# Kernel tuning notes

Measured on AMD Instinct MI355X. Metric: run time of the kernel, lower is better.

The kernel has to match this reference:

```python
import jax, jax.numpy as jnp
import numpy as np

N_NODES = 100000
N_EDGES = 1600000
IN_CH = 128
OUT_CH = 128


def setup_inputs() -> dict:
    key = jax.random.key(0)
    k1, k2, k3, k4, k5, k6 = jax.random.split(key, 6)
    x = jax.random.normal(k1, (N_NODES, IN_CH), dtype=jnp.float32)
    weight = jax.random.normal(k2, (IN_CH, OUT_CH), dtype=jnp.float32) * (1.0 / np.sqrt(IN_CH))
    bias = jax.random.uniform(k3, (OUT_CH,), dtype=jnp.float32)
    edge_row = jax.random.randint(k4, (N_EDGES,), 0, N_NODES, dtype=jnp.int64)
    edge_col = jax.random.randint(k5, (N_EDGES,), 0, N_NODES, dtype=jnp.int64)
    edge_weight = jax.random.uniform(k6, (N_EDGES,), dtype=jnp.float32)
    return {"x": x, "weight": weight, "bias": bias,
            "edge_row": edge_row, "edge_col": edge_col, "edge_weight": edge_weight}


def reference(x, weight, bias, edge_row, edge_col, edge_weight):
    # Dense transform: [N, in] @ [in, out] -> [N, out]
    h = x @ weight
    # SpMM: out[r] = sum_e w_e * h[c_e] for edges (r, c) -- gather + scatter-add
    msgs = edge_weight[:, None] * h[edge_col]          # [E, out]
    agg = jax.ops.segment_sum(msgs, edge_row, num_segments=N_NODES)  # [N, out]
    return agg + bias
```

## Files before the change

kernel.cpp:

```cpp
#include <hip/hip_runtime.h>

#define N_NODES 100000
#define N_EDGES_MAX 1600000
#define IN_CH 128
#define OUT_CH 128
#define NB 391
#define BLK_E 2048
#define NBLK_P 800
#define CAP_LDS 5120

typedef __attribute__((ext_vector_type(8))) short bf16x8_t;
typedef __attribute__((ext_vector_type(4))) float f32x4_t;

constexpr size_t align_up(size_t x) { return (x + 255) & ~size_t(255); }
constexpr size_t H_OFF     = 0;
constexpr size_t H_SZ      = (size_t)N_NODES * OUT_CH * 2;
constexpr size_t BREC_OFF  = align_up(H_OFF + H_SZ);
constexpr size_t BREC_SZ   = (size_t)N_EDGES_MAX * 8;
constexpr size_t SREC_OFF  = align_up(BREC_OFF + BREC_SZ);
constexpr size_t BLK_OFF   = align_up(SREC_OFF + BREC_SZ);
constexpr size_t BLK_SZ    = (size_t)NB * NBLK_P * 4;
constexpr size_t BTOT_OFF  = align_up(BLK_OFF + BLK_SZ);
constexpr size_t BTOT_SZ   = (size_t)NB * 4;
constexpr size_t BBASE_OFF = align_up(BTOT_OFF + BTOT_SZ);
constexpr size_t BBASE_SZ  = (size_t)(NB + 1) * 4;
constexpr size_t RS_OFF    = align_up(BBASE_OFF + BBASE_SZ);
constexpr size_t RS_SZ     = (size_t)(N_NODES + 1) * 4;
constexpr size_t WS_NEED   = RS_OFF + RS_SZ;

__device__ __forceinline__ unsigned short f2bf(float f) {
    unsigned u = __float_as_uint(f);
    return (unsigned short)((u + 0x7FFFu + ((u >> 16) & 1u)) >> 16);
}
__device__ __forceinline__ float bf2f(unsigned short b) {
    return __uint_as_float((unsigned)b << 16);
}
__device__ __forceinline__ float bflo(unsigned u) { return __uint_as_float(u << 16); }
__device__ __forceinline__ float bfhi(unsigned u) { return __uint_as_float(u & 0xFFFF0000u); }

__device__ __forceinline__ void accum8(float4& a0, float4& a1, const uint4 hv,
                                       const float wt) {
    a0.x += wt * bflo(hv.x); a0.y += wt * bfhi(hv.x);
    a0.z += wt * bflo(hv.y); a0.w += wt * bfhi(hv.y);
    a1.x += wt * bflo(hv.z); a1.y += wt * bfhi(hv.z);
    a1.z += wt * bflo(hv.w); a1.w += wt * bfhi(hv.w);
}

__global__ __launch_bounds__(256) void gemm_mfma(const float* __restrict__ x,
                                                 const float* __restrict__ W,
                                                 unsigned short* __restrict__ h) {
    __shared__ unsigned short WTl[128 * 136];
    const int t = threadIdx.x;

    const float4* W4 = (const float4*)W;
#pragma unroll
    for (int i = 0; i < 16; ++i) {
        const int idx = t + 256 * i;
        float4 v = W4[idx];
        const int base = idx * 4;
        const int k = base >> 7;
        const int c = base & 127;
        WTl[(c + 0) * 136 + k] = f2bf(v.x);
        WTl[(c + 1) * 136 + k] = f2bf(v.y);
        WTl[(c + 2) * 136 + k] = f2bf(v.z);
        WTl[(c + 3) * 136 + k] = f2bf(v.w);
    }
    __syncthreads();

    const int wv = t >> 6;
    const int l  = t & 63;
    const int lr = l & 15;
    const int lk = (l >> 4) * 8;
    const long rbase = (long)blockIdx.x * 64 + wv * 16;

    f32x4_t acc[8];
#pragma unroll
    for (int i = 0; i < 8; ++i) acc[i] = (f32x4_t){0.f, 0.f, 0.f, 0.f};

    long arow = rbase + lr;
    if (arow >= N_NODES) arow = N_NODES - 1;
    const float4* xr = (const float4*)(x + arow * IN_CH);

    for (int kc = 0; kc < 128; kc += 32) {
        float4 f0 = xr[(kc + lk) >> 2];
        float4 f1 = xr[((kc + lk) >> 2) + 1];
        bf16x8_t a;
        a[0] = (short)f2bf(f0.x); a[1] = (short)f2bf(f0.y);
        a[2] = (short)f2bf(f0.z); a[3] = (short)f2bf(f0.w);
        a[4] = (short)f2bf(f1.x); a[5] = (short)f2bf(f1.y);
        a[6] = (short)f2bf(f1.z); a[7] = (short)f2bf(f1.w);
#pragma unroll
        for (int ct = 0; ct < 8; ++ct) {
            bf16x8_t b = *(const bf16x8_t*)&WTl[(ct * 16 + lr) * 136 + kc + lk];
            acc[ct] = __builtin_amdgcn_mfma_f32_16x16x32_bf16(a, b, acc[ct], 0, 0, 0);
        }
    }

    const int r0 = (l >> 4) * 4;
#pragma unroll
    for (int ct = 0; ct < 8; ++ct) {
        const int col = ct * 16 + lr;
#pragma unroll
        for (int reg = 0; reg < 4; ++reg) {
            long r = rbase + r0 + reg;
            if (r < N_NODES) h[r * OUT_CH + col] = f2bf(acc[ct][reg]);
        }
    }
}

__global__ __launch_bounds__(256) void bucket_hist(const int* __restrict__ erow,
                                                   unsigned* __restrict__ blkcnt,
                                                   int n) {
    __shared__ unsigned cnt[NB];
    const int t = threadIdx.x, p = blockIdx.x;
    for (int i = t; i < NB; i += 256) cnt[i] = 0u;
    __syncthreads();
    const int e0 = p * BLK_E;
#pragma unroll
    for (int j = 0; j < 8; ++j) {
        int e = e0 + j * 256 + t;
        if (e < n) atomicAdd(&cnt[(unsigned)erow[e] >> 8], 1u);
    }
    __syncthreads();
    for (int i = t; i < NB; i += 256) blkcnt[(size_t)i * NBLK_P + p] = cnt[i];
}

__global__ __launch_bounds__(256) void scan_col(unsigned* __restrict__ blkcnt,
                                                unsigned* __restrict__ btotal,
                                                int nblk) {
    __shared__ unsigned part[256];
    const int b = blockIdx.x, t = threadIdx.x;
    unsigned* col = blkcnt + (size_t)b * NBLK_P;
    unsigned v[4];
    unsigned sum = 0;
    const int p0 = t * 4;
#pragma unroll
    for (int j = 0; j < 4; ++j) {
        int p = p0 + j;
        v[j] = (p < nblk) ? col[p] : 0u;
        sum += v[j];
    }
    part[t] = sum;
    __syncthreads();
    for (int off = 1; off < 256; off <<= 1) {
        unsigned a = (t >= off) ? part[t - off] : 0u;
        __syncthreads();
        part[t] += a;
        __syncthreads();
    }
    unsigned excl = part[t] - sum;
#pragma unroll
    for (int j = 0; j < 4; ++j) {
        int p = p0 + j;
        if (p < nblk) { unsigned tv = v[j]; col[p] = excl; excl += tv; }
    }
    if (t == 255) btotal[b] = part[255];
}

__global__ __launch_bounds__(512) void scan_buckets(const unsigned* __restrict__ btotal,
                                                    unsigned* __restrict__ bbase,
                                                    unsigned* __restrict__ row_start,
                                                    int n_edges) {
    __shared__ unsigned s[512];
    const int t = threadIdx.x;
    unsigned v = (t < NB) ? btotal[t] : 0u;
    s[t] = v;
    __syncthreads();
    for (int off = 1; off < 512; off <<= 1) {
        unsigned a = (t >= off) ? s[t - off] : 0u;
        __syncthreads();
        s[t] += a;
        __syncthreads();
    }
    if (t < NB) bbase[t] = s[t] - v;
    if (t == 0) {
        bbase[NB] = (unsigned)n_edges;
        row_start[N_NODES] = (unsigned)n_edges;
    }
}

__global__ __launch_bounds__(256) void bucket_scatter(const int* __restrict__ erow,
                                                      const int* __restrict__ ecol,
                                                      const float* __restrict__ ew,
                                                      const unsigned* __restrict__ blkbase,
                                                      const unsigned* __restrict__ bbase,
                                                      uint2* __restrict__ brec,
                                                      int n) {
    __shared__ unsigned cnt[NB];
    __shared__ unsigned basec[NB];
    const int t = threadIdx.x, p = blockIdx.x;
    for (int i = t; i < NB; i += 256) {
        cnt[i] = 0u;
        basec[i] = bbase[i] + blkbase[(size_t)i * NBLK_P + p];
    }
    __syncthreads();
    const int e0 = p * BLK_E;
#pragma unroll
    for (int j = 0; j < 8; ++j) {
        int e = e0 + j * 256 + t;
        if (e < n) {
            unsigned r = (unsigned)erow[e];
            unsigned c = (unsigned)ecol[e];
            float w = ew[e];
            unsigned bk = r >> 8;
            unsigned rank = atomicAdd(&cnt[bk], 1u);
            brec[basec[bk] + rank] =
                make_uint2(((r & 255u) << 17) | c, __float_as_uint(w));
        }
    }
}

__global__ __launch_bounds__(256) void row_scatter(const uint2* __restrict__ brec,
                                                   const unsigned* __restrict__ bbase,
                                                   unsigned* __restrict__ row_start,
                                                   uint2* __restrict__ srec) {
    __shared__ unsigned hist[256], sc[256], cur[256];
    __shared__ uint2 recs[CAP_LDS];
    const int b = blockIdx.x, t = threadIdx.x;
    const unsigned s = bbase[b], e = bbase[b + 1];
    const unsigned m = e - s;
    hist[t] = 0u;
    __syncthreads();
    const bool fits = (m <= CAP_LDS);
    if (fits) {
        for (unsigned i = t; i < m; i += 256) {
            uint2 rc = brec[s + i];
            recs[i] = rc;
            atomicAdd(&hist[rc.x >> 17], 1u);
        }
    } else {
        for (unsigned i = t; i < m; i += 256)
            atomicAdd(&hist[brec[s + i].x >> 17], 1u);
    }
    __syncthreads();
    unsigned v = hist[t];
    sc[t] = v;
    __syncthreads();
    for (int off = 1; off < 256; off <<= 1) {
        unsigned a = (t >= off) ? sc[t - off] : 0u;
        __syncthreads();
        sc[t] += a;
        __syncthreads();
    }
    const unsigned gpos = s + sc[t] - v;
    const int grow = b * 256 + t;
    if (grow < N_NODES) row_start[grow] = gpos;
    cur[t] = gpos;
    __syncthreads();
    if (fits) {
        for (unsigned i = t; i < m; i += 256) {
            uint2 rc = recs[i];
            unsigned pos = atomicAdd(&cur[rc.x >> 17], 1u);
            srec[pos] = make_uint2(rc.x & 0x1FFFFu, rc.y);
        }
    } else {
        for (unsigned i = t; i < m; i += 256) {
            uint2 rc = brec[s + i];
            unsigned pos = atomicAdd(&cur[rc.x >> 17], 1u);
            srec[pos] = make_uint2(rc.x & 0x1FFFFu, rc.y);
        }
    }
}

__global__ __launch_bounds__(256) void aggregate(const unsigned short* __restrict__ h,
                                                 const uint2* __restrict__ srec,
                                                 const unsigned* __restrict__ row_start,
                                                 const float* __restrict__ bias,
                                                 float* __restrict__ out) {
    const int t = threadIdx.x, lane = t & 15;
    const int r = blockIdx.x * 16 + (t >> 4);
    if (r >= N_NODES) return;
    const unsigned s = row_start[r], e = row_start[r + 1];

    const float4* b4 = (const float4*)bias;
    float4 a0 = b4[lane * 2];
    float4 a1 = b4[lane * 2 + 1];

    const uint4* h16 = (const uint4*)h;

    unsigned i = s;
    for (; i + 4 <= e; i += 4) {
        uint2 r0 = srec[i];
        uint2 r1 = srec[i + 1];
        uint2 r2 = srec[i + 2];
        uint2 r3 = srec[i + 3];
        uint4 v0 = h16[(size_t)r0.x * 16 + lane];
        uint4 v1 = h16[(size_t)r1.x * 16 + lane];
        uint4 v2 = h16[(size_t)r2.x * 16 + lane];
        uint4 v3 = h16[(size_t)r3.x * 16 + lane];
        accum8(a0, a1, v0, __uint_as_float(r0.y));
        accum8(a0, a1, v1, __uint_as_float(r1.y));
        accum8(a0, a1, v2, __uint_as_float(r2.y));
        accum8(a0, a1, v3, __uint_as_float(r3.y));
    }
    for (; i < e; ++i) {
        uint2 rc = srec[i];
        uint4 vv = h16[(size_t)rc.x * 16 + lane];
        accum8(a0, a1, vv, __uint_as_float(rc.y));
    }

    float4* o = (float4*)(out + (size_t)r * OUT_CH + lane * 8);
    o[0] = a0;
    o[1] = a1;
}

__global__ __launch_bounds__(256) void gemm_xw(const float* __restrict__ x,
                                               const float* __restrict__ W,
                                               unsigned short* __restrict__ h) {
    __shared__ float Wl[128 * 128];
    __shared__ float Xl[32 * 128];
    const int t = threadIdx.x;
    const float4* W4 = (const float4*)W;
    float4* Wl4 = (float4*)Wl;
#pragma unroll
    for (int i = 0; i < 16; ++i) Wl4[t + 256 * i] = W4[t + 256 * i];
    const long rbase = (long)blockIdx.x * 32;
    const float4* x4 = (const float4*)(x + rbase * IN_CH);
    float4* Xl4 = (float4*)Xl;
#pragma unroll
    for (int i = 0; i < 4; ++i) Xl4[t + 256 * i] = x4[t + 256 * i];
    __syncthreads();
    const int tx = t & 31;
    const int ty = t >> 5;
    float acc[4][4];
#pragma unroll
    for (int i = 0; i < 4; ++i)
#pragma unroll
        for (int j = 0; j < 4; ++j) acc[i][j] = 0.f;
    for (int k = 0; k < 128; ++k) {
        float4 w = *(const float4*)&Wl[k * 128 + tx * 4];
        float xv[4];
#pragma unroll
        for (int i = 0; i < 4; ++i) xv[i] = Xl[(ty * 4 + i) * 128 + k];
#pragma unroll
        for (int i = 0; i < 4; ++i) {
            acc[i][0] += xv[i] * w.x;
            acc[i][1] += xv[i] * w.y;
            acc[i][2] += xv[i] * w.z;
            acc[i][3] += xv[i] * w.w;
        }
    }
#pragma unroll
    for (int i = 0; i < 4; ++i) {
        long r = rbase + ty * 4 + i;
        ushort4 o;
        o.x = f2bf(acc[i][0]); o.y = f2bf(acc[i][1]);
        o.z = f2bf(acc[i][2]); o.w = f2bf(acc[i][3]);
        *(ushort4*)&h[r * OUT_CH + tx * 4] = o;
    }
}

__global__ __launch_bounds__(256) void init_bias(float* __restrict__ out,
                                                 const float* __restrict__ bias) {
    int idx = blockIdx.x * 256 + threadIdx.x;
    float4 b = ((const float4*)bias)[idx & 31];
    ((float4*)out)[idx] = b;
}

__global__ __launch_bounds__(256) void spmm_scatter(const unsigned short* __restrict__ h,
                                                    const int* __restrict__ erow,
                                                    const int* __restrict__ ecol,
                                                    const float* __restrict__ ew,
                                                    float* __restrict__ out,
                                                    int n_edges) {
    const int t = threadIdx.x;
    const int lane = t & 31;
    const int e = blockIdx.x * 8 + (t >> 5);
    if (e >= n_edges) return;
    const int r = erow[e];
    const int c = ecol[e];
    const float w = ew[e];
    ushort4 hv = ((const ushort4*)(h + (size_t)c * OUT_CH))[lane];
    float* o = out + (size_t)r * OUT_CH + lane * 4;
    atomicAdd(o + 0, w * bf2f(hv.x));
    atomicAdd(o + 1, w * bf2f(hv.y));
    atomicAdd(o + 2, w * bf2f(hv.z));
    atomicAdd(o + 3, w * bf2f(hv.w));
}

extern "C" void kernel_launch(void* const* d_in, const int* in_sizes, int n_in,
                              void* d_out, int out_size, void* d_ws, size_t ws_size,
                              hipStream_t stream) {
    const float* x    = (const float*)d_in[0];
    const float* W    = (const float*)d_in[1];
    const float* bias = (const float*)d_in[2];
    const int*   erow = (const int*)d_in[3];
    const int*   ecol = (const int*)d_in[4];
    const float* ew   = (const float*)d_in[5];
    float* out = (float*)d_out;
    const int n_edges = in_sizes[3];

    char* ws = (char*)d_ws;
    unsigned short* h  = (unsigned short*)(ws + H_OFF);
    uint2*    brec     = (uint2*)(ws + BREC_OFF);
    uint2*    srec     = (uint2*)(ws + SREC_OFF);
    unsigned* blkcnt   = (unsigned*)(ws + BLK_OFF);
    unsigned* btotal   = (unsigned*)(ws + BTOT_OFF);
    unsigned* bbase    = (unsigned*)(ws + BBASE_OFF);
    unsigned* rowstart = (unsigned*)(ws + RS_OFF);

    const int nblk = (n_edges + BLK_E - 1) / BLK_E;
    if (ws_size >= WS_NEED && n_edges <= N_EDGES_MAX) {
        gemm_mfma<<<(N_NODES + 63) / 64, 256, 0, stream>>>(x, W, h);
        bucket_hist<<<nblk, 256, 0, stream>>>(erow, blkcnt, n_edges);
        scan_col<<<NB, 256, 0, stream>>>(blkcnt, btotal, nblk);
        scan_buckets<<<1, 512, 0, stream>>>(btotal, bbase, rowstart, n_edges);
        bucket_scatter<<<nblk, 256, 0, stream>>>(erow, ecol, ew, blkcnt, bbase,
                                                 brec, n_edges);
        row_scatter<<<NB, 256, 0, stream>>>(brec, bbase, rowstart, srec);
        aggregate<<<(N_NODES + 15) / 16, 256, 0, stream>>>(h, srec, rowstart,
                                                           bias, out);
    } else {
        gemm_xw<<<N_NODES / 32, 256, 0, stream>>>(x, W, h);
        init_bias<<<(N_NODES * 32) / 256, 256, 0, stream>>>(out, bias);
        spmm_scatter<<<(n_edges + 7) / 8, 256, 0, stream>>>(h, erow, ecol, ew,
                                                            out, n_edges);
    }
}
```

Baseline: 146.8 us.

## Fuse GEMM with bucket histogram and fold bucket scan into last-block scan_col

Merges the MFMA GEMM and the edge bucket histogram into one launch, with blocks split by index, so the two independent stages run concurrently. It also removes the single-block scan_buckets kernel: the last scan_col block to finish, detected through an atomic done counter, performs the bucket-total scan. This cuts two kernel launches and their inter-kernel gaps. In exchange the fused kernel reserves GEMM-sized LDS for histogram blocks too, and the design relies on a threadfence plus atomic last-block pattern, with the counter reset inside the histogram blocks.

```diff
diff --git a/kernel.cpp b/kernel.cpp
--- a/kernel.cpp
+++ b/kernel.cpp
@@ -8,6 +8,7 @@
 #define BLK_E 2048
 #define NBLK_P 800
 #define CAP_LDS 5120
+#define G_GEMM ((N_NODES + 63) / 64)
 
 typedef __attribute__((ext_vector_type(8))) short bf16x8_t;
 typedef __attribute__((ext_vector_type(4))) float f32x4_t;
@@ -26,7 +27,8 @@
 constexpr size_t BBASE_SZ  = (size_t)(NB + 1) * 4;
 constexpr size_t RS_OFF    = align_up(BBASE_OFF + BBASE_SZ);
 constexpr size_t RS_SZ     = (size_t)(N_NODES + 1) * 4;
-constexpr size_t WS_NEED   = RS_OFF + RS_SZ;
+constexpr size_t DONE_OFF  = align_up(RS_OFF + RS_SZ);
+constexpr size_t WS_NEED   = DONE_OFF + 256;
 
 __device__ __forceinline__ unsigned short f2bf(float f) {
     unsigned u = __float_as_uint(f);
@@ -46,89 +48,97 @@
     a1.z += wt * bflo(hv.w); a1.w += wt * bfhi(hv.w);
 }
 
-__global__ __launch_bounds__(256) void gemm_mfma(const float* __restrict__ x,
+__global__ __launch_bounds__(256) void gemm_hist(const float* __restrict__ x,
                                                  const float* __restrict__ W,
-                                                 unsigned short* __restrict__ h) {
+                                                 unsigned short* __restrict__ h,
+                                                 const int* __restrict__ erow,
+                                                 unsigned* __restrict__ blkcnt,
+                                                 unsigned* __restrict__ done,
+                                                 int n) {
     __shared__ unsigned short WTl[128 * 136];
+    __shared__ unsigned cnt[NB];
     const int t = threadIdx.x;
 
-    const float4* W4 = (const float4*)W;
-#pragma unroll
-    for (int i = 0; i < 16; ++i) {
-        const int idx = t + 256 * i;
-        float4 v = W4[idx];
-        const int base = idx * 4;
-        const int k = base >> 7;
-        const int c = base & 127;
-        WTl[(c + 0) * 136 + k] = f2bf(v.x);
-        WTl[(c + 1) * 136 + k] = f2bf(v.y);
-        WTl[(c + 2) * 136 + k] = f2bf(v.z);
-        WTl[(c + 3) * 136 + k] = f2bf(v.w);
-    }
-    __syncthreads();
-
-    const int wv = t >> 6;
-    const int l  = t & 63;
-    const int lr = l & 15;
-    const int lk = (l >> 4) * 8;
-    const long rbase = (long)blockIdx.x * 64 + wv * 16;
-
-    f32x4_t acc[8];
-#pragma unroll
-    for (int i = 0; i < 8; ++i) acc[i] = (f32x4_t){0.f, 0.f, 0.f, 0.f};
-
-    long arow = rbase + lr;
-    if (arow >= N_NODES) arow = N_NODES - 1;
-    const float4* xr = (const float4*)(x + arow * IN_CH);
-
-    for (int kc = 0; kc < 128; kc += 32) {
-        float4 f0 = xr[(kc + lk) >> 2];
-        float4 f1 = xr[((kc + lk) >> 2) + 1];
-        bf16x8_t a;
-        a[0] = (short)f2bf(f0.x); a[1] = (short)f2bf(f0.y);
-        a[2] = (short)f2bf(f0.z); a[3] = (short)f2bf(f0.w);
-        a[4] = (short)f2bf(f1.x); a[5] = (short)f2bf(f1.y);
-        a[6] = (short)f2bf(f1.z); a[7] = (short)f2bf(f1.w);
+    if ((int)blockIdx.x < G_GEMM) {
+        const float4* W4 = (const float4*)W;
+#pragma unroll
+        for (int i = 0; i < 16; ++i) {
+            const int idx = t + 256 * i;
+            float4 v = W4[idx];
+            const int base = idx * 4;
+            const int k = base >> 7;
+            const int c = base & 127;
+            WTl[(c + 0) * 136 + k] = f2bf(v.x);
+            WTl[(c + 1) * 136 + k] = f2bf(v.y);
+            WTl[(c + 2) * 136 + k] = f2bf(v.z);
+            WTl[(c + 3) * 136 + k] = f2bf(v.w);
+        }
+        __syncthreads();
+
+        const int wv = t >> 6;
+        const int l  = t & 63;
+        const int lr = l & 15;
+        const int lk = (l >> 4) * 8;
+        const long rbase = (long)blockIdx.x * 64 + wv * 16;
+
+        f32x4_t acc[8];
+#pragma unroll
+        for (int i = 0; i < 8; ++i) acc[i] = (f32x4_t){0.f, 0.f, 0.f, 0.f};
+
+        long arow = rbase + lr;
+        if (arow >= N_NODES) arow = N_NODES - 1;
+        const float4* xr = (const float4*)(x + arow * IN_CH);
+
+        for (int kc = 0; kc < 128; kc += 32) {
+            float4 f0 = xr[(kc + lk) >> 2];
+            float4 f1 = xr[((kc + lk) >> 2) + 1];
+            bf16x8_t a;
+            a[0] = (short)f2bf(f0.x); a[1] = (short)f2bf(f0.y);
+            a[2] = (short)f2bf(f0.z); a[3] = (short)f2bf(f0.w);
+            a[4] = (short)f2bf(f1.x); a[5] = (short)f2bf(f1.y);
+            a[6] = (short)f2bf(f1.z); a[7] = (short)f2bf(f1.w);
+#pragma unroll
+            for (int ct = 0; ct < 8; ++ct) {
+                bf16x8_t b = *(const bf16x8_t*)&WTl[(ct * 16 + lr) * 136 + kc + lk];
+                acc[ct] = __builtin_amdgcn_mfma_f32_16x16x32_bf16(a, b, acc[ct], 0, 0, 0);
+            }
+        }
+
+        const int r0 = (l >> 4) * 4;
 #pragma unroll
         for (int ct = 0; ct < 8; ++ct) {
-            bf16x8_t b = *(const bf16x8_t*)&WTl[(ct * 16 + lr) * 136 + kc + lk];
-            acc[ct] = __builtin_amdgcn_mfma_f32_16x16x32_bf16(a, b, acc[ct], 0, 0, 0);
-        }
-    }
-
-    const int r0 = (l >> 4) * 4;
-#pragma unroll
-    for (int ct = 0; ct < 8; ++ct) {
-        const int col = ct * 16 + lr;
-#pragma unroll
-        for (int reg = 0; reg < 4; ++reg) {
-            long r = rbase + r0 + reg;
-            if (r < N_NODES) h[r * OUT_CH + col] = f2bf(acc[ct][reg]);
-        }
-    }
-}
-
-__global__ __launch_bounds__(256) void bucket_hist(const int* __restrict__ erow,
-                                                   unsigned* __restrict__ blkcnt,
-                                                   int n) {
-    __shared__ unsigned cnt[NB];
-    const int t = threadIdx.x, p = blockIdx.x;
-    for (int i = t; i < NB; i += 256) cnt[i] = 0u;
-    __syncthreads();
-    const int e0 = p * BLK_E;
-#pragma unroll
-    for (int j = 0; j < 8; ++j) {
-        int e = e0 + j * 256 + t;
-        if (e < n) atomicAdd(&cnt[(unsigned)erow[e] >> 8], 1u);
-    }
-    __syncthreads();
-    for (int i = t; i < NB; i += 256) blkcnt[(size_t)i * NBLK_P + p] = cnt[i];
+            const int col = ct * 16 + lr;
+#pragma unroll
+            for (int reg = 0; reg < 4; ++reg) {
+                long r = rbase + r0 + reg;
+                if (r < N_NODES) h[r * OUT_CH + col] = f2bf(acc[ct][reg]);
+            }
+        }
+    } else {
+        const int p = (int)blockIdx.x - G_GEMM;
+        if (p == 0 && t == 0) *done = 0u;
+        for (int i = t; i < NB; i += 256) cnt[i] = 0u;
+        __syncthreads();
+        const int e0 = p * BLK_E;
+#pragma unroll
+        for (int j = 0; j < 8; ++j) {
+            int e = e0 + j * 256 + t;
+            if (e < n) atomicAdd(&cnt[(unsigned)erow[e] >> 8], 1u);
+        }
+        __syncthreads();
+        for (int i = t; i < NB; i += 256) blkcnt[(size_t)i * NBLK_P + p] = cnt[i];
+    }
 }
 
 __global__ __launch_bounds__(256) void scan_col(unsigned* __restrict__ blkcnt,
                                                 unsigned* __restrict__ btotal,
-                                                int nblk) {
+                                                unsigned* __restrict__ bbase,
+                                                unsigned* __restrict__ row_start,
+                                                unsigned* __restrict__ done,
+                                                int nblk, int n_edges) {
     __shared__ unsigned part[256];
+    __shared__ unsigned sb[NB];
+    __shared__ bool amlast;
     const int b = blockIdx.x, t = threadIdx.x;
     unsigned* col = blkcnt + (size_t)b * NBLK_P;
     unsigned v[4];
@@ -155,24 +165,30 @@
         if (p < nblk) { unsigned tv = v[j]; col[p] = excl; excl += tv; }
     }
     if (t == 255) btotal[b] = part[255];
-}
-
-__global__ __launch_bounds__(512) void scan_buckets(const unsigned* __restrict__ btotal,
-                                                    unsigned* __restrict__ bbase,
-                                                    unsigned* __restrict__ row_start,
-                                                    int n_edges) {
-    __shared__ unsigned s[512];
-    const int t = threadIdx.x;
-    unsigned v = (t < NB) ? btotal[t] : 0u;
-    s[t] = v;
-    __syncthreads();
-    for (int off = 1; off < 512; off <<= 1) {
-        unsigned a = (t >= off) ? s[t - off] : 0u;
-        __syncthreads();
-        s[t] += a;
-        __syncthreads();
-    }
-    if (t < NB) bbase[t] = s[t] - v;
+    __threadfence();
+    __syncthreads();
+    if (t == 0) amlast = (atomicAdd(done, 1u) == NB - 1u);
+    __syncthreads();
+    if (!amlast) return;
+
+    __threadfence();
+    for (int i = t; i < NB; i += 256) sb[i] = btotal[i];
+    __syncthreads();
+    const int q0 = t * 2;
+    unsigned u0 = (q0 < NB) ? sb[q0] : 0u;
+    unsigned u1 = (q0 + 1 < NB) ? sb[q0 + 1] : 0u;
+    unsigned s2 = u0 + u1;
+    part[t] = s2;
+    __syncthreads();
+    for (int off = 1; off < 256; off <<= 1) {
+        unsigned a = (t >= off) ? part[t - off] : 0u;
+        __syncthreads();
+        part[t] += a;
+        __syncthreads();
+    }
+    unsigned ex = part[t] - s2;
+    if (q0 < NB) bbase[q0] = ex;
+    if (q0 + 1 < NB) bbase[q0 + 1] = ex + u0;
     if (t == 0) {
         bbase[NB] = (unsigned)n_edges;
         row_start[N_NODES] = (unsigned)n_edges;
@@ -398,13 +414,14 @@
     unsigned* btotal   = (unsigned*)(ws + BTOT_OFF);
     unsigned* bbase    = (unsigned*)(ws + BBASE_OFF);
     unsigned* rowstart = (unsigned*)(ws + RS_OFF);
+    unsigned* done     = (unsigned*)(ws + DONE_OFF);
 
     const int nblk = (n_edges + BLK_E - 1) / BLK_E;
     if (ws_size >= WS_NEED && n_edges <= N_EDGES_MAX) {
-        gemm_mfma<<<(N_NODES + 63) / 64, 256, 0, stream>>>(x, W, h);
-        bucket_hist<<<nblk, 256, 0, stream>>>(erow, blkcnt, n_edges);
-        scan_col<<<NB, 256, 0, stream>>>(blkcnt, btotal, nblk);
-        scan_buckets<<<1, 512, 0, stream>>>(btotal, bbase, rowstart, n_edges);
+        gemm_hist<<<G_GEMM + nblk, 256, 0, stream>>>(x, W, h, erow, blkcnt,
+                                                     done, n_edges);
+        scan_col<<<NB, 256, 0, stream>>>(blkcnt, btotal, bbase, rowstart, done,
+                                         nblk, n_edges);
         bucket_scatter<<<nblk, 256, 0, stream>>>(erow, ecol, ew, blkcnt, bbase,
                                                  brec, n_edges);
         row_scatter<<<NB, 256, 0, stream>>>(brec, bbase, rowstart, srec);
```

Measured after the change: 179.9 us. 1.23x slower.
